# Kernel optimization log

Measured on AMD Instinct MI355X. Metric: run time of the kernel, lower is better.

Reference implementation:

```python
import jax, jax.numpy as jnp
import numpy as np
import math

N = 100000
E = 1600000
D = 256          # input_size
H = 64           # head_size = input_size // n_heads = 256 // 4


def setup_inputs() -> dict:
    key = jax.random.key(0)
    k1, k2, k3, k4, k5 = jax.random.split(key, 5)
    X = jax.random.normal(k1, (N, D), dtype=jnp.float32)
    edge_index = jax.random.randint(k2, (2, E), 0, N, dtype=jnp.int64)
    # Linear(input_size, head_size, bias=False) weights, stored as [D, H] so Q = X @ Wq
    s = 1.0 / math.sqrt(D)
    Wq = jax.random.uniform(k3, (D, H), dtype=jnp.float32, minval=-s, maxval=s)
    Wk = jax.random.uniform(k4, (D, H), dtype=jnp.float32, minval=-s, maxval=s)
    Wv = jax.random.uniform(k5, (D, H), dtype=jnp.float32, minval=-s, maxval=s)
    return {"X": X, "Wq": Wq, "Wk": Wk, "Wv": Wv, "edge_index": edge_index}


def reference(X, Wq, Wk, Wv, edge_index):
    dk = math.sqrt(H)
    Q = X @ Wq  # [N, H]
    K = X @ Wk
    V = X @ Wv
    src = edge_index[0]  # row of sparse matrix -> softmax segment (dim=1 softmax)
    dst = edge_index[1]  # column -> neighbor supplying K/V
    scores = jnp.sum(Q[src] * K[dst], axis=-1) / dk  # [E]
    # per-row (per src node) stable softmax over edges
    m = jax.ops.segment_max(scores, src, num_segments=N)          # [N], -inf for empty rows
    m = jnp.where(jnp.isfinite(m), m, 0.0)
    e = jnp.exp(scores - m[src])                                   # [E]
    denom = jax.ops.segment_sum(e, src, num_segments=N)            # [N]
    alpha = e / jnp.maximum(denom[src], 1e-38)                     # [E]
    # scatter-weighted V aggregation: out[i] = sum_{(i,j) in edges} alpha_ij * V[j]
    out = jax.ops.segment_sum(alpha[:, None] * V[dst], src, num_segments=N)  # [N, H]
    return out
```

## Files before the change

### kernel.cpp

```cpp
#include <hip/hip_runtime.h>

typedef unsigned short u16;
typedef unsigned int u32;
typedef short short8 __attribute__((ext_vector_type(8)));
typedef float f32x4 __attribute__((ext_vector_type(4)));
typedef u32 u32x4 __attribute__((ext_vector_type(4)));

__device__ __forceinline__ u16 f2bf(float f) {
    union { float f; u32 i; } c; c.f = f;
    u32 i = c.i;
    return (u16)((i + 0x7FFFu + ((i >> 16) & 1u)) >> 16);
}
__device__ __forceinline__ float bf2f(u16 u) {
    union { u32 i; float f; } c; c.i = ((u32)u) << 16; return c.f;
}
__device__ __forceinline__ void bf2x(u32 p, float& lo, float& hi) {
    union { u32 i; float f; } a, b;
    a.i = p << 16; b.i = p & 0xFFFF0000u;
    lo = a.f; hi = b.f;
}
__device__ __forceinline__ u32 cvtpk_bf16(float lo, float hi) {
    u32 r;
    asm("v_cvt_pk_bf16_f32 %0, %1, %2" : "=v"(r) : "v"(lo), "v"(hi));
    return r;
}

__global__ void wfrag_kernel(const float* __restrict__ Wq,
                             const float* __restrict__ Wk,
                             const float* __restrict__ Wv,
                             u16* __restrict__ wf)
{
    int idx = blockIdx.x * 256 + threadIdx.x;
    if (idx >= 12 * 8 * 64) return;
    int lane = idx & 63;
    int s = (idx >> 6) & 7;
    int t = idx >> 9;
    int n = t * 16 + (lane & 15);
    const float* Wsrc = (n < 64) ? Wq : ((n < 128) ? Wk : Wv);
    int col = n & 63;
    int kbase = s * 32 + (lane >> 4) * 8;
    u16 o[8];
#pragma unroll
    for (int j = 0; j < 8; ++j) o[j] = f2bf(Wsrc[(size_t)(kbase + j) * 64 + col]);
    *(short8*)(wf + (size_t)idx * 8) = *(const short8*)o;
}

#define TM 32
__global__ __launch_bounds__(256, 2) void qkv_mfma(
    const float* __restrict__ X, const u16* __restrict__ wf,
    float* __restrict__ Qs, u16* __restrict__ Ksb, u16* __restrict__ Vsb,
    int N, int NT)
{
    __shared__ float xs[TM * 256];

    const int tid  = threadIdx.x;
    const int lane = tid & 63;
    const int wave = tid >> 6;
    const int m    = lane & 15;
    const int quad = lane >> 4;
    const int t0   = wave * 3;

    const short8* wfp = (const short8*)wf;
    short8 bfr0[8], bfr1[8], bfr2[8];
#pragma unroll
    for (int s = 0; s < 8; ++s) {
        bfr0[s] = wfp[(size_t)((t0 + 0) * 8 + s) * 64 + lane];
        bfr1[s] = wfp[(size_t)((t0 + 1) * 8 + s) * 64 + lane];
        bfr2[s] = wfp[(size_t)((t0 + 2) * 8 + s) * 64 + lane];
    }

    for (int tile = blockIdx.x; tile < NT; tile += gridDim.x) {
#pragma unroll
        for (int it = 0; it < 8; ++it) {
            int c0  = (it * 4 + wave) * 64;
            int c   = c0 + lane;
            int row = c >> 6;
            int sblk = (c & 63) ^ (row & 7);
            int arow = tile * TM + row;
            if (arow >= N) arow = N - 1;
            const float* g = X + (size_t)arow * 256 + sblk * 4;
            float* l = xs + c0 * 4;
            __builtin_amdgcn_global_load_lds(
                (const __attribute__((address_space(1))) void*)g,
                (__attribute__((address_space(3))) void*)l, 16, 0, 0);
        }
        __syncthreads();

        f32x4 acc[2][3];
#pragma unroll
        for (int rb = 0; rb < 2; ++rb)
#pragma unroll
            for (int tt = 0; tt < 3; ++tt) acc[rb][tt] = (f32x4)0.f;

#pragma unroll
        for (int rb = 0; rb < 2; ++rb) {
            const int row = rb * 16 + m;
            const float* xrow = xs + row * 256;
            const int sw = m & 7;
#pragma unroll
            for (int s = 0; s < 8; ++s) {
                int B0 = quad * 2 + s * 8;
                float4 a0 = *(const float4*)(xrow + ((B0)     ^ sw) * 4);
                float4 a1 = *(const float4*)(xrow + ((B0 + 1) ^ sw) * 4);
                union { u32x4 u; short8 s8; } af;
                af.u.x = cvtpk_bf16(a0.x, a0.y);
                af.u.y = cvtpk_bf16(a0.z, a0.w);
                af.u.z = cvtpk_bf16(a1.x, a1.y);
                af.u.w = cvtpk_bf16(a1.z, a1.w);
                acc[rb][0] = __builtin_amdgcn_mfma_f32_16x16x32_bf16(af.s8, bfr0[s], acc[rb][0], 0, 0, 0);
                acc[rb][1] = __builtin_amdgcn_mfma_f32_16x16x32_bf16(af.s8, bfr1[s], acc[rb][1], 0, 0, 0);
                acc[rb][2] = __builtin_amdgcn_mfma_f32_16x16x32_bf16(af.s8, bfr2[s], acc[rb][2], 0, 0, 0);
            }
        }

#pragma unroll
        for (int rb = 0; rb < 2; ++rb) {
            int rbase = tile * TM + rb * 16 + quad * 4;
#pragma unroll
            for (int tt = 0; tt < 3; ++tt) {
                int t = t0 + tt;
                int col = (t & 3) * 16 + m;
#pragma unroll
                for (int r = 0; r < 4; ++r) {
                    int rr = rbase + r;
                    if (rr >= N) continue;
                    float v = acc[rb][tt][r];
                    if (t < 4)      Qs [(size_t)rr * 64 + col] = v;
                    else if (t < 8) Ksb[(size_t)rr * 64 + col] = f2bf(v);
                    else            Vsb[(size_t)rr * 64 + col] = f2bf(v);
                }
            }
        }
        __syncthreads();
    }
}


__global__ __launch_bounds__(256) void count_kernel(
    const int* __restrict__ src, int* __restrict__ bsize,
    int E, int N, int NB, int chunk)
{
    __shared__ int cnt[512];
    for (int i = threadIdx.x; i < 512; i += 256) cnt[i] = 0;
    __syncthreads();
    int lo = blockIdx.x * chunk;
    int hi = min(E, lo + chunk);
    for (int e = lo + (int)threadIdx.x; e < hi; e += 256) {
        int s = src[e];
        if ((unsigned)s < (unsigned)N) atomicAdd(&cnt[s >> 8], 1);
    }
    __syncthreads();
    for (int b = threadIdx.x; b < NB; b += 256)
        if (cnt[b]) atomicAdd(&bsize[b], cnt[b]);
}

__global__ __launch_bounds__(512) void scan391_kernel(
    const int* __restrict__ bsize, int* __restrict__ bbase,
    int* __restrict__ cursor, int* __restrict__ row_ptr_N, int NB)
{
    __shared__ int sd[512];
    int t = threadIdx.x;
    int v = (t < NB) ? bsize[t] : 0;
    sd[t] = v;
    __syncthreads();
    for (int off = 1; off < 512; off <<= 1) {
        int x = (t >= off) ? sd[t - off] : 0;
        __syncthreads();
        sd[t] += x;
        __syncthreads();
    }
    if (t < NB) {
        int excl = sd[t] - v;
        bbase[t] = excl;
        cursor[t] = excl;
        if (t == NB - 1) {
            bbase[NB] = sd[t];
            *row_ptr_N = sd[t];
        }
    }
}

__global__ __launch_bounds__(256) void scatter_pairs_kernel(
    const int* __restrict__ src, const int* __restrict__ dst,
    int* __restrict__ cursor, int2* __restrict__ pairs,
    int E, int N, int NB, int chunk)
{
    __shared__ int cnt[512];
    __shared__ int basei[512];
    for (int i = threadIdx.x; i < 512; i += 256) cnt[i] = 0;
    __syncthreads();
    int lo = blockIdx.x * chunk;
    int hi = min(E, lo + chunk);
    for (int e = lo + (int)threadIdx.x; e < hi; e += 256) {
        int s = src[e];
        if ((unsigned)s < (unsigned)N) atomicAdd(&cnt[s >> 8], 1);
    }
    __syncthreads();
    for (int b = threadIdx.x; b < NB; b += 256)
        basei[b] = cnt[b] ? atomicAdd(&cursor[b], cnt[b]) : 0;
    __syncthreads();
    for (int i = threadIdx.x; i < 512; i += 256) cnt[i] = 0;
    __syncthreads();
    for (int e = lo + (int)threadIdx.x; e < hi; e += 256) {
        int s = src[e];
        if ((unsigned)s >= (unsigned)N) continue;
        int d = dst[e];
        if ((unsigned)d >= (unsigned)N) d = 0;
        int bk = s >> 8;
        int p = basei[bk] + atomicAdd(&cnt[bk], 1);
        pairs[p] = make_int2(s, d);
    }
}

#define MAXB 6144
__global__ __launch_bounds__(256) void sort_bucket_kernel(
    const int2* __restrict__ pairs, const int* __restrict__ bbase,
    int* __restrict__ row_ptr, int* __restrict__ sorted_dst, int N)
{
    __shared__ int deg[256];
    __shared__ int off[256];
    __shared__ int cur[256];
    __shared__ int ldst[MAXB];

    int bk = blockIdx.x;
    int n0 = bk * 256;
    int nn = min(256, N - n0);
    int base = bbase[bk];
    int size = bbase[bk + 1] - base;
    int t = threadIdx.x;

    deg[t] = 0;
    __syncthreads();
    for (int i = t; i < size; i += 256)
        atomicAdd(&deg[pairs[base + i].x & 255], 1);
    __syncthreads();
    off[t] = deg[t];
    __syncthreads();
    for (int s = 1; s < 256; s <<= 1) {
        int x = (t >= s) ? off[t - s] : 0;
        __syncthreads();
        off[t] += x;
        __syncthreads();
    }
    int excl = off[t] - deg[t];
    cur[t] = excl;
    if (t < nn) row_ptr[n0 + t] = base + excl;
    __syncthreads();
    int cap = min(size, MAXB);
    for (int i = t; i < size; i += 256) {
        int2 pr = pairs[base + i];
        int p = atomicAdd(&cur[pr.x & 255], 1);
        if (p < MAXB) ldst[p] = pr.y;
    }
    __syncthreads();
    for (int i = t; i < cap; i += 256)
        sorted_dst[base + i] = ldst[i];
    for (int i = cap + t; i < size; i += 256)
        sorted_dst[base + i] = 0;
}

__global__ __launch_bounds__(256) void attn_csr(
    const float* __restrict__ Qs, const u16* __restrict__ Ksb,
    const u16* __restrict__ Vsb, const int* __restrict__ row_ptr,
    const int* __restrict__ sdst, float* __restrict__ out, int N)
{
    int wid = (int)((blockIdx.x * 256 + threadIdx.x) >> 6);
    if (wid >= N) return;
    int lane = threadIdx.x & 63;
    int sub = lane >> 3;
    int sl  = lane & 7;

    const float* qp = Qs + (size_t)wid * 64 + sl * 8;
    float4 q0 = *(const float4*)(qp);
    float4 q1 = *(const float4*)(qp + 4);

    int beg = row_ptr[wid];
    int end = row_ptr[wid + 1];

    float l = 0.f;
    float a0 = 0.f, a1 = 0.f, a2 = 0.f, a3 = 0.f;
    float a4 = 0.f, a5 = 0.f, a6 = 0.f, a7 = 0.f;

    for (int j = beg; j < end; j += 8) {
        int e = j + sub;
        bool valid = (e < end);
        int d = sdst[valid ? e : beg];

        uint4 kr = *(const uint4*)(Ksb + (size_t)d * 64 + sl * 8);
        float k0, k1, k2, k3, k4, k5, k6, k7;
        bf2x(kr.x, k0, k1); bf2x(kr.y, k2, k3);
        bf2x(kr.z, k4, k5); bf2x(kr.w, k6, k7);

        float p = q0.x * k0 + q0.y * k1 + q0.z * k2 + q0.w * k3
                + q1.x * k4 + q1.y * k5 + q1.z * k6 + q1.w * k7;
        p += __shfl_xor(p, 1);
        p += __shfl_xor(p, 2);
        p += __shfl_xor(p, 4);

        float pe = __expf(p * 0.125f);

        uint4 vr = *(const uint4*)(Vsb + (size_t)d * 64 + sl * 8);
        float v0, v1, v2, v3, v4, v5, v6, v7;
        bf2x(vr.x, v0, v1); bf2x(vr.y, v2, v3);
        bf2x(vr.z, v4, v5); bf2x(vr.w, v6, v7);

        if (valid) {
            l += pe;
            a0 += pe * v0; a1 += pe * v1; a2 += pe * v2; a3 += pe * v3;
            a4 += pe * v4; a5 += pe * v5; a6 += pe * v6; a7 += pe * v7;
        }
    }

#pragma unroll
    for (int off = 8; off <= 32; off <<= 1) {
        l  += __shfl_xor(l, off);
        a0 += __shfl_xor(a0, off); a1 += __shfl_xor(a1, off);
        a2 += __shfl_xor(a2, off); a3 += __shfl_xor(a3, off);
        a4 += __shfl_xor(a4, off); a5 += __shfl_xor(a5, off);
        a6 += __shfl_xor(a6, off); a7 += __shfl_xor(a7, off);
    }

    if (sub == 0) {
        float inv = (l > 0.f) ? (1.f / l) : 0.f;
        float* op = out + (size_t)wid * 64 + sl * 8;
        *(float4*)(op)     = make_float4(a0 * inv, a1 * inv, a2 * inv, a3 * inv);
        *(float4*)(op + 4) = make_float4(a4 * inv, a5 * inv, a6 * inv, a7 * inv);
    }
}

extern "C" void kernel_launch(void* const* d_in, const int* in_sizes, int n_in,
                              void* d_out, int out_size, void* d_ws, size_t ws_size,
                              hipStream_t stream)
{
    const float* X  = (const float*)d_in[0];
    const float* Wq = (const float*)d_in[1];
    const float* Wk = (const float*)d_in[2];
    const float* Wv = (const float*)d_in[3];
    const int*   ei = (const int*)d_in[4];

    const int N = in_sizes[0] / 256;
    const int E = in_sizes[4] / 2;
    const int* src = ei;
    const int* dst = ei + E;
    const int NB = (N + 255) >> 8;

    char* w = (char*)d_ws;
    float* Qs = (float*)w;      w += (size_t)N * 64 * sizeof(float);
    u16* Ksb = (u16*)w;         w += (size_t)N * 64 * sizeof(u16);
    u16* Vsb = (u16*)w;         w += (size_t)N * 64 * sizeof(u16);
    int2* pairs = (int2*)w;     w += (size_t)E * sizeof(int2);
    int* sorted_dst = (int*)w;  w += (size_t)E * sizeof(int);
    int* row_ptr = (int*)w;     w += (size_t)(N + 1) * sizeof(int);
    int* bsize = (int*)w;       w += (size_t)(NB + 1) * sizeof(int);
    int* bbase = (int*)w;       w += (size_t)(NB + 1) * sizeof(int);
    int* cursor = (int*)w;      w += (size_t)(NB + 1) * sizeof(int);
    u16* wf = (u16*)w;          w += (size_t)12 * 8 * 64 * 8 * sizeof(u16);

    hipMemsetAsync(bsize, 0, (size_t)(NB + 1) * sizeof(int), stream);

    const int B1 = 160;
    const int chunk = (E + B1 - 1) / B1;
    const int NT = (N + TM - 1) / TM;

    wfrag_kernel<<<24, 256, 0, stream>>>(Wq, Wk, Wv, wf);
    qkv_mfma<<<768, 256, 0, stream>>>(X, wf, Qs, Ksb, Vsb, N, NT);

    count_kernel<<<B1, 256, 0, stream>>>(src, bsize, E, N, NB, chunk);
    scan391_kernel<<<1, 512, 0, stream>>>(bsize, bbase, cursor, row_ptr + N, NB);
    scatter_pairs_kernel<<<B1, 256, 0, stream>>>(src, dst, cursor, pairs, E, N, NB, chunk);
    sort_bucket_kernel<<<NB, 256, 0, stream>>>(pairs, bbase, row_ptr, sorted_dst, N);

    attn_csr<<<(N * 64 + 255) / 256, 256, 0, stream>>>(
        Qs, Ksb, Vsb, row_ptr, sorted_dst, (float*)d_out, N);
}
```

Baseline: 339.1 us.

## Interleave K/V rows and process each node with an 8-lane subgroup

K and V are now stored interleaved in one bf16 buffer, so each neighbor's K and V sit in one 256-byte row. The attention kernel maps one 8-lane subgroup per source node instead of one full wave, which removes the cross-subgroup shuffle reduction and the lanes wasted on rows with few edges. Each subgroup walks its edges one by one and software-prefetches the next neighbor's K/V. The trade-off is less memory-level parallelism per node and divergence between subgroups with different degrees in the same wave.

Result: no change. 337.8 us (-0.4%).

```diff
diff --git a/kernel.cpp b/kernel.cpp
--- a/kernel.cpp
+++ b/kernel.cpp
@@ -48,7 +48,7 @@
 #define TM 32
 __global__ __launch_bounds__(256, 2) void qkv_mfma(
     const float* __restrict__ X, const u16* __restrict__ wf,
-    float* __restrict__ Qs, u16* __restrict__ Ksb, u16* __restrict__ Vsb,
+    float* __restrict__ Qs, u16* __restrict__ KVsb,
     int N, int NT)
 {
     __shared__ float xs[TM * 256];
@@ -125,9 +125,9 @@
                     int rr = rbase + r;
                     if (rr >= N) continue;
                     float v = acc[rb][tt][r];
-                    if (t < 4)      Qs [(size_t)rr * 64 + col] = v;
-                    else if (t < 8) Ksb[(size_t)rr * 64 + col] = f2bf(v);
-                    else            Vsb[(size_t)rr * 64 + col] = f2bf(v);
+                    if (t < 4)      Qs  [(size_t)rr * 64  + col]      = v;
+                    else if (t < 8) KVsb[(size_t)rr * 128 + col]      = f2bf(v);
+                    else            KVsb[(size_t)rr * 128 + 64 + col] = f2bf(v);
                 }
             }
         }
@@ -260,72 +260,66 @@
 }
 
 __global__ __launch_bounds__(256) void attn_csr(
-    const float* __restrict__ Qs, const u16* __restrict__ Ksb,
-    const u16* __restrict__ Vsb, const int* __restrict__ row_ptr,
-    const int* __restrict__ sdst, float* __restrict__ out, int N)
-{
-    int wid = (int)((blockIdx.x * 256 + threadIdx.x) >> 6);
-    if (wid >= N) return;
-    int lane = threadIdx.x & 63;
-    int sub = lane >> 3;
-    int sl  = lane & 7;
-
-    const float* qp = Qs + (size_t)wid * 64 + sl * 8;
+    const float* __restrict__ Qs, const u16* __restrict__ KVsb,
+    const int* __restrict__ row_ptr, const int* __restrict__ sdst,
+    float* __restrict__ out, int N)
+{
+    int sg = (int)((blockIdx.x * 256 + threadIdx.x) >> 3);
+    if (sg >= N) return;
+    int sl = threadIdx.x & 7;
+
+    const float* qp = Qs + (size_t)sg * 64 + sl * 8;
     float4 q0 = *(const float4*)(qp);
     float4 q1 = *(const float4*)(qp + 4);
 
-    int beg = row_ptr[wid];
-    int end = row_ptr[wid + 1];
+    int beg = row_ptr[sg];
+    int end = row_ptr[sg + 1];
 
     float l = 0.f;
     float a0 = 0.f, a1 = 0.f, a2 = 0.f, a3 = 0.f;
     float a4 = 0.f, a5 = 0.f, a6 = 0.f, a7 = 0.f;
 
-    for (int j = beg; j < end; j += 8) {
-        int e = j + sub;
-        bool valid = (e < end);
-        int d = sdst[valid ? e : beg];
-
-        uint4 kr = *(const uint4*)(Ksb + (size_t)d * 64 + sl * 8);
-        float k0, k1, k2, k3, k4, k5, k6, k7;
-        bf2x(kr.x, k0, k1); bf2x(kr.y, k2, k3);
-        bf2x(kr.z, k4, k5); bf2x(kr.w, k6, k7);
-
-        float p = q0.x * k0 + q0.y * k1 + q0.z * k2 + q0.w * k3
-                + q1.x * k4 + q1.y * k5 + q1.z * k6 + q1.w * k7;
-        p += __shfl_xor(p, 1);
-        p += __shfl_xor(p, 2);
-        p += __shfl_xor(p, 4);
-
-        float pe = __expf(p * 0.125f);
-
-        uint4 vr = *(const uint4*)(Vsb + (size_t)d * 64 + sl * 8);
-        float v0, v1, v2, v3, v4, v5, v6, v7;
-        bf2x(vr.x, v0, v1); bf2x(vr.y, v2, v3);
-        bf2x(vr.z, v4, v5); bf2x(vr.w, v6, v7);
-
-        if (valid) {
+    if (beg < end) {
+        int d0 = sdst[beg];
+        const u16* kv = KVsb + (size_t)d0 * 128 + sl * 8;
+        uint4 kr = *(const uint4*)(kv);
+        uint4 vr = *(const uint4*)(kv + 64);
+
+        for (int j = beg; j < end; ++j) {
+            int jn = j + 1;
+            int dn = (jn < end) ? sdst[jn] : d0;
+            const u16* kvn = KVsb + (size_t)dn * 128 + sl * 8;
+            uint4 krn = *(const uint4*)(kvn);
+            uint4 vrn = *(const uint4*)(kvn + 64);
+
+            float k0, k1, k2, k3, k4, k5, k6, k7;
+            bf2x(kr.x, k0, k1); bf2x(kr.y, k2, k3);
+            bf2x(kr.z, k4, k5); bf2x(kr.w, k6, k7);
+
+            float p = q0.x * k0 + q0.y * k1 + q0.z * k2 + q0.w * k3
+                    + q1.x * k4 + q1.y * k5 + q1.z * k6 + q1.w * k7;
+            p += __shfl_xor(p, 1);
+            p += __shfl_xor(p, 2);
+            p += __shfl_xor(p, 4);
+
+            float pe = __expf(p * 0.125f);
+
+            float v0, v1, v2, v3, v4, v5, v6, v7;
+            bf2x(vr.x, v0, v1); bf2x(vr.y, v2, v3);
+            bf2x(vr.z, v4, v5); bf2x(vr.w, v6, v7);
+
             l += pe;
             a0 += pe * v0; a1 += pe * v1; a2 += pe * v2; a3 += pe * v3;
             a4 += pe * v4; a5 += pe * v5; a6 += pe * v6; a7 += pe * v7;
-        }
-    }
-
-#pragma unroll
-    for (int off = 8; off <= 32; off <<= 1) {
-        l  += __shfl_xor(l, off);
-        a0 += __shfl_xor(a0, off); a1 += __shfl_xor(a1, off);
-        a2 += __shfl_xor(a2, off); a3 += __shfl_xor(a3, off);
-        a4 += __shfl_xor(a4, off); a5 += __shfl_xor(a5, off);
-        a6 += __shfl_xor(a6, off); a7 += __shfl_xor(a7, off);
-    }
-
-    if (sub == 0) {
-        float inv = (l > 0.f) ? (1.f / l) : 0.f;
-        float* op = out + (size_t)wid * 64 + sl * 8;
-        *(float4*)(op)     = make_float4(a0 * inv, a1 * inv, a2 * inv, a3 * inv);
-        *(float4*)(op + 4) = make_float4(a4 * inv, a5 * inv, a6 * inv, a7 * inv);
-    }
+
+            kr = krn; vr = vrn;
+        }
+    }
+
+    float inv = (l > 0.f) ? (1.f / l) : 0.f;
+    float* op = out + (size_t)sg * 64 + sl * 8;
+    *(float4*)(op)     = make_float4(a0 * inv, a1 * inv, a2 * inv, a3 * inv);
+    *(float4*)(op + 4) = make_float4(a4 * inv, a5 * inv, a6 * inv, a7 * inv);
 }
 
 extern "C" void kernel_launch(void* const* d_in, const int* in_sizes, int n_in,
@@ -346,8 +340,7 @@
 
     char* w = (char*)d_ws;
     float* Qs = (float*)w;      w += (size_t)N * 64 * sizeof(float);
-    u16* Ksb = (u16*)w;         w += (size_t)N * 64 * sizeof(u16);
-    u16* Vsb = (u16*)w;         w += (size_t)N * 64 * sizeof(u16);
+    u16* KVsb = (u16*)w;        w += (size_t)N * 128 * sizeof(u16);
     int2* pairs = (int2*)w;     w += (size_t)E * sizeof(int2);
     int* sorted_dst = (int*)w;  w += (size_t)E * sizeof(int);
     int* row_ptr = (int*)w;     w += (size_t)(N + 1) * sizeof(int);
@@ -363,13 +356,13 @@
     const int NT = (N + TM - 1) / TM;
 
     wfrag_kernel<<<24, 256, 0, stream>>>(Wq, Wk, Wv, wf);
-    qkv_mfma<<<768, 256, 0, stream>>>(X, wf, Qs, Ksb, Vsb, N, NT);
+    qkv_mfma<<<768, 256, 0, stream>>>(X, wf, Qs, KVsb, N, NT);
 
     count_kernel<<<B1, 256, 0, stream>>>(src, bsize, E, N, NB, chunk);
     scan391_kernel<<<1, 512, 0, stream>>>(bsize, bbase, cursor, row_ptr + N, NB);
     scatter_pairs_kernel<<<B1, 256, 0, stream>>>(src, dst, cursor, pairs, E, N, NB, chunk);
     sort_bucket_kernel<<<NB, 256, 0, stream>>>(pairs, bbase, row_ptr, sorted_dst, N);
 
-    attn_csr<<<(N * 64 + 255) / 256, 256, 0, stream>>>(
-        Qs, Ksb, Vsb, row_ptr, sorted_dst, (float*)d_out, N);
-}
+    attn_csr<<<(N * 8 + 255) / 256, 256, 0, stream>>>(
+        Qs, KVsb, row_ptr, sorted_dst, (float*)d_out, N);
+}
```
